# Optimization experiments

Measured on AMD Instinct MI355X. Metric: run time of the kernel, lower is better.

Reference implementation:

```python
import jax, jax.numpy as jnp
import numpy as np

STEPS, K, NEW_PTS, GDIM, HDIM = 10, 64, 1152, 256, 128


def setup_inputs() -> dict:
    key = jax.random.key(0)
    ks = jax.random.split(key, 24)
    def w(k, shape):
        return jax.random.normal(k, shape, dtype=jnp.float32) * 0.02
    inp = {
        'points': jax.random.normal(ks[0], (4, 4096, 3), dtype=jnp.float32),
        'gt': jax.random.normal(ks[1], (4, 4096, 3), dtype=jnp.float32),
        # PointNet encoder: 3->64->128->256 (stored [in,out])
        'enc_w1': w(ks[2], (3, 64)),   'enc_b1': jnp.zeros((64,), jnp.float32),
        'enc_w2': w(ks[3], (64, 128)), 'enc_b2': jnp.zeros((128,), jnp.float32),
        'enc_w3': w(ks[4], (128, GDIM)), 'enc_b3': jnp.zeros((GDIM,), jnp.float32),
        # Attention MLP: (3+256+128)->128->1
        'att_w1': w(ks[5], (3 + GDIM + HDIM, 128)), 'att_b1': jnp.zeros((128,), jnp.float32),
        'att_w2': w(ks[6], (128, 1)), 'att_b2': jnp.zeros((1,), jnp.float32),
        # LSTMCell: input 256+3+3=262, hidden 128, gates i,f,g,o
        'lstm_wih': w(ks[7], (GDIM + 6, 4 * HDIM)), 'lstm_whh': w(ks[8], (HDIM, 4 * HDIM)),
        'lstm_bih': jnp.zeros((4 * HDIM,), jnp.float32), 'lstm_bhh': jnp.zeros((4 * HDIM,), jnp.float32),
        # Refiner: 128->128->new_points*3
        'ref_w1': w(ks[9], (HDIM, 128)), 'ref_b1': jnp.zeros((128,), jnp.float32),
        'ref_w2': w(ks[10], (128, NEW_PTS * 3)), 'ref_b2': jnp.zeros((NEW_PTS * 3,), jnp.float32),
    }
    return inp


def _chamfer_sq(x, y):
    # x: [B,N,3], y: [B,M,3]; squared-L2 chamfer, batch-mean (pytorch3d norm=2)
    d2 = (jnp.sum(x * x, -1)[:, :, None] + jnp.sum(y * y, -1)[:, None, :]
          - 2.0 * jnp.einsum('bnd,bmd->bnm', x, y))  # [B,N,M]
    cd = jnp.mean(jnp.min(d2, axis=2), axis=1) + jnp.mean(jnp.min(d2, axis=1), axis=1)
    return jnp.mean(cd)


def _forward(points, gt, enc_w1, enc_b1, enc_w2, enc_b2, enc_w3, enc_b3,
             att_w1, att_b1, att_w2, att_b2,
             lstm_wih, lstm_whh, lstm_bih, lstm_bhh,
             ref_w1, ref_b1, ref_w2, ref_b2):
    B, N0, _ = points.shape
    h = jnp.zeros((B, HDIM), points.dtype)
    c = jnp.zeros((B, HDIM), points.dtype)
    canvas = points
    for _ in range(STEPS):
        # PointNet encoder + max-pool -> global feature [B,GDIM]
        f = jax.nn.relu(canvas @ enc_w1 + enc_b1)
        f = jax.nn.relu(f @ enc_w2 + enc_b2)
        f = f @ enc_w3 + enc_b3
        gfeat = jnp.max(f, axis=1)
        # attention-weighted centroid
        N = canvas.shape[1]
        ctx = jnp.concatenate([
            canvas,
            jnp.broadcast_to(gfeat[:, None, :], (B, N, GDIM)),
            jnp.broadcast_to(h[:, None, :], (B, N, HDIM)),
        ], axis=-1)
        scores = (jax.nn.relu(ctx @ att_w1 + att_b1) @ att_w2 + att_b2)[..., 0]  # [B,N]
        alpha = jax.nn.softmax(scores, axis=1)
        center = jnp.einsum('bn,bnd->bd', alpha, canvas)
        # brute-force KNN around center + gather
        dist = jnp.linalg.norm(canvas - center[:, None, :], axis=-1)  # [B,N]
        _, idx = jax.lax.top_k(-dist, K)  # smallest K
        patch = jnp.take_along_axis(canvas, idx[:, :, None], axis=1)  # [B,K,3]
        patch_feat = jnp.mean(patch - center[:, None, :], axis=1)  # [B,3]
        # LSTM cell (gate order i,f,g,o)
        lstm_in = jnp.concatenate([gfeat, center, patch_feat], axis=1)
        gates = lstm_in @ lstm_wih + lstm_bih + h @ lstm_whh + lstm_bhh
        gi, gf, gg, go = jnp.split(gates, 4, axis=1)
        c = jax.nn.sigmoid(gf) * c + jax.nn.sigmoid(gi) * jnp.tanh(gg)
        h = jax.nn.sigmoid(go) * jnp.tanh(c)
        # refine: generate new patch points around center
        new_pts = (jax.nn.relu(h @ ref_w1 + ref_b1) @ ref_w2 + ref_b2)
        new_pts = new_pts.reshape(B, NEW_PTS, 3) * 0.02 + center[:, None, :]
        canvas = jnp.concatenate([canvas, new_pts], axis=1)
    p_input = canvas[:, :N0, :]
    p_new = canvas[:, N0:, :]
    total_loss = 0.1 * _chamfer_sq(p_input, gt) + 1.0 * _chamfer_sq(p_new, gt)
    return total_loss


def reference(points, gt, enc_w1, enc_b1, enc_w2, enc_b2, enc_w3, enc_b3,
              att_w1, att_b1, att_w2, att_b2,
              lstm_wih, lstm_whh, lstm_bih, lstm_bhh,
              ref_w1, ref_b1, ref_w2, ref_b2):
    return _forward(points, gt, enc_w1, enc_b1, enc_w2, enc_b2, enc_w3, enc_b3,
                    att_w1, att_b1, att_w2, att_b2,
                    lstm_wih, lstm_whh, lstm_bih, lstm_bhh,
                    ref_w1, ref_b1, ref_w2, ref_b2)
```

## Files before the change

kernel.cpp:

```cpp
#include <hip/hip_runtime.h>
#include <math.h>

#define BB 4
#define N0 4096
#define NEWP 1152
#define GD 256
#define HD 128
#define KSEL 64
#define NSTEPS 10
#define NMAX (N0 + NSTEPS*NEWP)
#define NNEW (NSTEPS*NEWP)

#define OFF_CANVAS 0
#define OFF_MINAB  (OFF_CANVAS + BB*NMAX*3)
#define OFF_MINCD  (OFF_MINAB + 2*BB*N0)
#define OFF_GMAX   (OFF_MINCD + BB*NNEW + BB*N0)
#define OFF_H      (OFF_GMAX + BB*GD)
#define OFF_C      (OFF_H + 2*BB*HD)
#define OFF_ACC    (OFF_C + 2*BB*HD)
#define OFF_CENTER (OFF_ACC + 16)
#define OFF_PART   (OFF_CENTER + 32)
#define OFF_GPART  (OFF_PART + BB*32*8)
#define WS_FLOATS  (OFF_GPART + 32*BB*512)

#define F1S 68
#define F2SD 132

__device__ __forceinline__ unsigned enc_f(float f){
  unsigned u = __float_as_uint(f);
  return (u & 0x80000000u) ? ~u : (u | 0x80000000u);
}
__device__ __forceinline__ float dec_f(unsigned e){
  unsigned u = (e & 0x80000000u) ? (e & 0x7fffffffu) : ~e;
  return __uint_as_float(u);
}
__device__ __forceinline__ float sigm(float x){ return 1.f/(1.f+expf(-x)); }

__device__ __forceinline__ float block_sum(float v, volatile float* red){
#pragma unroll
  for (int s=32;s>0;s>>=1) v += __shfl_down(v, s, 64);
  int lane = threadIdx.x & 63, w = threadIdx.x >> 6, nw = blockDim.x >> 6;
  __syncthreads();
  if (lane==0) red[w] = v;
  __syncthreads();
  if (w==0){
    float x = (lane < nw) ? red[lane] : 0.f;
#pragma unroll
    for (int s=8;s>0;s>>=1) x += __shfl_down(x, s, 64);
    if (lane==0) red[0] = x;
  }
  __syncthreads();
  float r = red[0];
  __syncthreads();
  return r;
}
__device__ __forceinline__ float block_max(float v, volatile float* red){
#pragma unroll
  for (int s=32;s>0;s>>=1) v = fmaxf(v, __shfl_down(v, s, 64));
  int lane = threadIdx.x & 63, w = threadIdx.x >> 6, nw = blockDim.x >> 6;
  __syncthreads();
  if (lane==0) red[w] = v;
  __syncthreads();
  if (w==0){
    float x = (lane < nw) ? red[lane] : -3.4e38f;
#pragma unroll
    for (int s=8;s>0;s>>=1) x = fmaxf(x, __shfl_down(x, s, 64));
    if (lane==0) red[0] = x;
  }
  __syncthreads();
  float r = red[0];
  __syncthreads();
  return r;
}

__device__ __forceinline__ void enc64(
    const float* __restrict__ sP, float* __restrict__ sF1, float* __restrict__ sF2,
    const float* __restrict__ w1, const float* __restrict__ b1,
    const float* __restrict__ w2, const float* __restrict__ b2,
    const float* __restrict__ w3, const float* __restrict__ b3,
    unsigned* __restrict__ gmax_b)
{
  int tid = threadIdx.x;
  int lane = tid & 63;
  int wv = __builtin_amdgcn_readfirstlane(tid >> 6);
#pragma unroll
  for (int k=0;k<8;k++){
    int pt = wv + 8*k;
    float p0 = sP[pt*3], p1 = sP[pt*3+1], p2 = sP[pt*3+2];
    float v = b1[lane] + p0*w1[lane] + p1*w1[64+lane] + p2*w1[128+lane];
    sF1[pt*F1S + lane] = fmaxf(v, 0.f);
  }
  __syncthreads();
  {
    float a[16];
    const float* b2p = b2 + wv*16;
#pragma unroll
    for (int k=0;k<16;k++) a[k] = b2p[k];
#pragma unroll
    for (int kk4=0; kk4<16; kk4++){
      float4 f4 = *(const float4*)&sF1[lane*F1S + kk4*4];
#pragma unroll
      for (int e=0;e<4;e++){
        float fk = ((const float*)&f4)[e];
        const float* wr = w2 + (kk4*4+e)*128 + wv*16;
#pragma unroll
        for (int k=0;k<16;k++) a[k] += fk*wr[k];
      }
    }
#pragma unroll
    for (int k=0;k<16;k++) sF2[lane*F2SD + wv*16 + k] = fmaxf(a[k], 0.f);
  }
  __syncthreads();
  {
    float a3[32];
    const float* b3p = b3 + wv*32;
#pragma unroll
    for (int d=0;d<32;d++) a3[d] = b3p[d];
#pragma unroll 8
    for (int k4=0; k4<32; k4++){
      float4 f4 = *(const float4*)&sF2[lane*F2SD + k4*4];
#pragma unroll
      for (int e=0;e<4;e++){
        float fk = ((const float*)&f4)[e];
        const float* wr = w3 + (k4*4+e)*256 + wv*32;
#pragma unroll
        for (int d=0;d<32;d++) a3[d] += fk*wr[d];
      }
    }
#pragma unroll
    for (int d=0;d<32;d++){
      float v = a3[d];
#pragma unroll
      for (int s=32;s>0;s>>=1) v = fmaxf(v, __shfl_down(v, s, 64));
      if (lane==0) atomicMax(&gmax_b[wv*32 + d], enc_f(v));
    }
  }
}

__global__ __launch_bounds__(512) void init_kernel(
    const float* __restrict__ points,
    float* __restrict__ canvas, unsigned* __restrict__ minAB,
    unsigned* __restrict__ minCD, unsigned* __restrict__ gmax,
    float* __restrict__ h, float* __restrict__ c)
{
  int gid = blockIdx.x*512 + threadIdx.x;
  if (gid < BB*N0*3){
    int b = gid/(N0*3), r = gid - b*(N0*3);
    canvas[(size_t)b*NMAX*3 + r] = points[gid];
  }
  if (gid < 2*BB*N0) minAB[gid] = 0xFFFFFFFFu;
  if (gid < BB*NNEW + BB*N0) minCD[gid] = 0xFFFFFFFFu;
  if (gid < BB*GD) gmax[gid] = 0u;
  if (gid < 2*BB*HD){ h[gid]=0.f; c[gid]=0.f; }
}

__global__ __launch_bounds__(512) void enc_kernel(
    const float* __restrict__ canvas,
    const float* __restrict__ w1, const float* __restrict__ b1,
    const float* __restrict__ w2, const float* __restrict__ b2,
    const float* __restrict__ w3, const float* __restrict__ b3,
    unsigned* __restrict__ gmax)
{
  __shared__ __align__(16) float sP[192];
  __shared__ __align__(16) float sF1[64*F1S];
  __shared__ __align__(16) float sF2[64*F2SD];
  int b = blockIdx.y, lg = blockIdx.x;
  int tid = threadIdx.x;
  if (tid < 192) sP[tid] = canvas[(size_t)b*NMAX*3 + (size_t)lg*192 + tid];
  __syncthreads();
  enc64(sP, sF1, sF2, w1, b1, w2, b2, w3, b3, gmax + b*GD);
}

__global__ __launch_bounds__(512) void sl_kernel(
    const float* __restrict__ canvas, const float* __restrict__ aw1,
    const float* __restrict__ ab1, const float* __restrict__ aw2,
    const float* __restrict__ ab2, const unsigned* __restrict__ gmax,
    const float* __restrict__ h_in,
    const float* __restrict__ wih, const float* __restrict__ whh,
    float* __restrict__ part, float* __restrict__ gpart, int N, int nch)
{
  __shared__ float sBatt[128];
  __shared__ float red[16];
  __shared__ float sV[BB][12];
  int blk = blockIdx.x;
  int tid = threadIdx.x;
  if (blk < 4*nch){
    int b = blk / nch, ch = blk - b*nch;
    if (tid < 128){
      float a = ab1[tid];
      for (int k=0;k<GD;k++) a += dec_f(gmax[b*GD+k]) * aw1[(3+k)*128 + tid];
      for (int k=0;k<HD;k++) a += h_in[b*HD+k] * aw1[(3+GD+k)*128 + tid];
      sBatt[tid] = a;
    }
    __syncthreads();
    int i = ch*512 + tid;
    bool act = i < N;
    float p0=0.f,p1=0.f,p2=0.f,s=-3.4e38f;
    if (act){
      const float* pp = canvas + (size_t)(b*NMAX + i)*3;
      p0=pp[0]; p1=pp[1]; p2=pp[2];
      s = ab2[0];
      for (int j=0;j<128;j++){
        float v = sBatt[j] + p0*aw1[j] + p1*aw1[128+j] + p2*aw1[256+j];
        s += fmaxf(v, 0.f)*aw2[j];
      }
    }
    float mb = block_max(s, red);
    float e = act ? expf(s - mb) : 0.f;
    float se = block_sum(e, red);
    float wx = block_sum(e*p0, red);
    float wy = block_sum(e*p1, red);
    float wz = block_sum(e*p2, red);
    if (tid==0){
      float* pr = part + (size_t)(b*32 + ch)*8;
      pr[0]=mb; pr[1]=se; pr[2]=wx; pr[3]=wy; pr[4]=wz;
    }
  } else {
    int cc = blk - 4*nch;
    if (tid < BB*12){
      int b = tid/12, j = tid - b*12;
      int r = cc*12 + j;
      sV[b][j] = (r < 256) ? dec_f(gmax[b*GD + r]) : h_in[b*HD + (r-256)];
    }
    __syncthreads();
    float a0=0.f,a1=0.f,a2=0.f,a3=0.f;
#pragma unroll
    for (int j=0;j<12;j++){
      int r = cc*12 + j;
      const float* wr = (r < 256) ? (wih + (size_t)r*512) : (whh + (size_t)(r-256)*512);
      float wvv = wr[tid];
      a0 += sV[0][j]*wvv; a1 += sV[1][j]*wvv;
      a2 += sV[2][j]*wvv; a3 += sV[3][j]*wvv;
    }
    float* gp = gpart + (size_t)cc*(BB*512);
    gp[0*512+tid]=a0; gp[1*512+tid]=a1; gp[2*512+tid]=a2; gp[3*512+tid]=a3;
  }
}

__global__ __launch_bounds__(1024) void stepA_kernel(
    const float* __restrict__ canvas, const float* __restrict__ part,
    float* __restrict__ centerpf, int N, int nch)
{
  __shared__ float red[16];
  __shared__ float sC[3];
  __shared__ unsigned cbufA[2][16];
  __shared__ unsigned cbufB[2][16];
  __shared__ int tieCnt;
  __shared__ int tieIdx[256];

  int b = blockIdx.x;
  int tid = threadIdx.x;
  int lane = tid & 63, wid = tid >> 6;
  const float* cv = canvas + (size_t)b*NMAX*3;

  float pm=-3.4e38f, pse=0.f, pwx=0.f, pwy=0.f, pwz=0.f;
  if (tid < nch){
    const float* pp = part + (size_t)(b*32 + tid)*8;
    pm=pp[0]; pse=pp[1]; pwx=pp[2]; pwy=pp[3]; pwz=pp[4];
  }
  float M = block_max(pm, red);
  float w = (tid < nch) ? expf(pm - M) : 0.f;
  float se = block_sum(pse*w, red);
  float wx = block_sum(pwx*w, red);
  float wy = block_sum(pwy*w, red);
  float wz = block_sum(pwz*w, red);
  if (tid==0){ sC[0]=wx/se; sC[1]=wy/se; sC[2]=wz/se; }
  __syncthreads();
  float cx=sC[0], cy=sC[1], cz=sC[2];
  if (tid<3) centerpf[b*3+tid] = sC[tid];

  unsigned ur[16];
#pragma unroll
  for (int q=0;q<16;q++){
    ur[q] = 0xFFFFFFFFu;
    int i = tid + q*1024;
    if (i < N){
      const float* p = cv + (size_t)i*3;
      float dx=p[0]-cx, dy=p[1]-cy, dz=p[2]-cz;
      ur[q] = __float_as_uint(dx*dx + dy*dy + dz*dz);
    }
  }

  unsigned T = 0u;
  int cntBelow = 0;
  int par = 0;
  {
    unsigned cand = 1u<<30;
    unsigned tc = 0;
#pragma unroll
    for (int q=0;q<16;q++) tc += (ur[q] < cand) ? 1u : 0u;
#pragma unroll
    for (int s=32;s>0;s>>=1) tc += __shfl_down(tc, s, 64);
    if (lane==0) cbufA[par][wid] = tc;
    __syncthreads();
    unsigned tot = 0;
#pragma unroll
    for (int i2=0;i2<16;i2++) tot += cbufA[par][i2];
    if ((int)tot < KSEL){ T = cand; cntBelow = (int)tot; }
    par ^= 1;
  }
  for (int bit=29; bit>=1; bit-=2){
    unsigned q1 = 1u<<(bit-1);
    unsigned c1 = T + q1, c2 = T + 2u*q1, c3 = T + 3u*q1;
    unsigned ta = 0, tb = 0;
#pragma unroll
    for (int q=0;q<16;q++){
      unsigned u = ur[q];
      ta += (u < c1 ? 1u : 0u) | (u < c2 ? 0x10000u : 0u);
      tb += (u < c3 ? 1u : 0u);
    }
#pragma unroll
    for (int s=32;s>0;s>>=1){ ta += __shfl_down(ta, s, 64); tb += __shfl_down(tb, s, 64); }
    if (lane==0){ cbufA[par][wid] = ta; cbufB[par][wid] = tb; }
    __syncthreads();
    unsigned sa = 0, sb = 0;
#pragma unroll
    for (int i2=0;i2<16;i2++){ sa += cbufA[par][i2]; sb += cbufB[par][i2]; }
    int n1 = (int)(sa & 0xFFFFu), n2 = (int)(sa >> 16), n3 = (int)sb;
    if (n3 < KSEL){ T = c3; cntBelow = n3; }
    else if (n2 < KSEL){ T = c2; cntBelow = n2; }
    else if (n1 < KSEL){ T = c1; cntBelow = n1; }
    par ^= 1;
  }
  int kneed = KSEL - cntBelow;

  if (tid==0) tieCnt = 0;
  __syncthreads();
  float sx=0.f, sy=0.f, sz=0.f;
#pragma unroll
  for (int q=0;q<16;q++){
    unsigned u = ur[q];
    if (u < T){
      const float* p = cv + (size_t)(tid + q*1024)*3;
      sx += p[0]; sy += p[1]; sz += p[2];
    } else if (u == T){
      int pos = atomicAdd(&tieCnt, 1);
      if (pos < 256) tieIdx[pos] = tid + q*1024;
    }
  }
  __syncthreads();
  sx = block_sum(sx, red);
  sy = block_sum(sy, red);
  sz = block_sum(sz, red);
  if (tid==0){
    int mm = tieCnt < 256 ? tieCnt : 256;
    for (int t=0;t<kneed;t++){
      int best=-1, bi=0x7fffffff;
      for (int q=0;q<mm;q++){ int v = tieIdx[q]; if (v < bi){ bi=v; best=q; } }
      if (best >= 0){
        tieIdx[best] = 0x7fffffff;
        const float* p = cv + (size_t)bi*3;
        sx += p[0]; sy += p[1]; sz += p[2];
      }
    }
    centerpf[16 + b*3 + 0] = sx/KSEL - cx;
    centerpf[16 + b*3 + 1] = sy/KSEL - cy;
    centerpf[16 + b*3 + 2] = sz/KSEL - cz;
  }
}

__global__ __launch_bounds__(512) void refine_enc_kernel(
    float* __restrict__ canvas, const float* __restrict__ gpart,
    const float* __restrict__ centerpf,
    const float* __restrict__ c_in, float* __restrict__ c_out,
    float* __restrict__ h_out,
    const float* __restrict__ wih,
    const float* __restrict__ bih, const float* __restrict__ bhh,
    const float* __restrict__ rw1, const float* __restrict__ rb1,
    const float* __restrict__ rw2, const float* __restrict__ rb2,
    const float* __restrict__ w1, const float* __restrict__ b1,
    const float* __restrict__ w2, const float* __restrict__ b2,
    const float* __restrict__ w3, const float* __restrict__ b3,
    unsigned* __restrict__ gmax, int N)
{
  __shared__ float sG[512];
  __shared__ float sH[HD];
  __shared__ float sRf[HD];
  __shared__ __align__(16) float sP[192];
  __shared__ __align__(16) float sF1[64*F1S];
  __shared__ __align__(16) float sF2[64*F2SD];
  int g = blockIdx.x, b = blockIdx.y;
  int tid = threadIdx.x;
  float cx = centerpf[b*3+0], cy = centerpf[b*3+1], cz = centerpf[b*3+2];
  float fx = centerpf[16+b*3+0], fy = centerpf[16+b*3+1], fz = centerpf[16+b*3+2];
  {
    float gg = bih[tid] + bhh[tid];
    for (int cc=0; cc<32; cc++) gg += gpart[(size_t)cc*(BB*512) + b*512 + tid];
    gg += cx*wih[(size_t)256*512+tid] + cy*wih[(size_t)257*512+tid] + cz*wih[(size_t)258*512+tid];
    gg += fx*wih[(size_t)259*512+tid] + fy*wih[(size_t)260*512+tid] + fz*wih[(size_t)261*512+tid];
    sG[tid] = gg;
  }
  __syncthreads();
  if (tid < HD){
    float gi=sG[tid], gf=sG[128+tid], gg2=sG[256+tid], go=sG[384+tid];
    float cn = sigm(gf)*c_in[b*HD+tid] + sigm(gi)*tanhf(gg2);
    float hn = sigm(go)*tanhf(cn);
    sH[tid] = hn;
    if (g==0){ c_out[b*HD+tid]=cn; h_out[b*HD+tid]=hn; }
  }
  __syncthreads();
  if (tid < HD){
    float a = rb1[tid];
    for (int k=0;k<HD;k++) a += sH[k]*rw1[k*HD + tid];
    sRf[tid] = fmaxf(a, 0.f);
  }
  __syncthreads();
  if (tid < 192){
    int o = g*192 + tid;
    float a = rb2[o];
    for (int k=0;k<HD;k++) a += sRf[k]*rw2[(size_t)k*(NEWP*3) + o];
    float val = a*0.02f + centerpf[b*3 + (tid%3)];
    sP[tid] = val;
    canvas[((size_t)b*NMAX + N)*3 + o] = val;
  }
  __syncthreads();
  enc64(sP, sF1, sF2, w1, b1, w2, b2, w3, b3, gmax + b*GD);
}

__global__ __launch_bounds__(512) void chamfer_kernel(
    const float* __restrict__ canvas, const float* __restrict__ gt,
    unsigned* __restrict__ minAB, unsigned* __restrict__ minCD)
{
  __shared__ float sy0[1024], sy1[1024], sy2[1024], sny[1024];
  int id = blockIdx.x;
  int dir, rem;
  if (id < 32){ dir=0; rem=id; }
  else if (id < 64){ dir=1; rem=id-32; }
  else if (id < 160){ dir=2; rem=id-64; }
  else { dir=3; rem=id-160; }
  int b, xb, yb;
  if (dir < 2){ b = rem>>3; int l = rem&7; xb = l>>2; yb = l&3; }
  else if (dir == 2){ b = rem/24; int l = rem%24; xb = l>>2; yb = l&3; }
  else { b = rem/24; int l = rem%24; xb = l/12; yb = l%12; }

  int Nx, Ny; const float* X; const float* Y; unsigned* mp;
  if (dir==0){      Nx=N0;   Ny=N0;   X=canvas+(size_t)b*NMAX*3;       Y=gt+(size_t)b*N0*3;            mp=minAB + b*N0; }
  else if (dir==1){ Nx=N0;   Ny=N0;   X=gt+(size_t)b*N0*3;             Y=canvas+(size_t)b*NMAX*3;      mp=minAB + BB*N0 + b*N0; }
  else if (dir==2){ Nx=NNEW; Ny=N0;   X=canvas+((size_t)b*NMAX+N0)*3;  Y=gt+(size_t)b*N0*3;            mp=minCD + b*NNEW; }
  else {            Nx=N0;   Ny=NNEW; X=gt+(size_t)b*N0*3;             Y=canvas+((size_t)b*NMAX+N0)*3; mp=minCD + BB*NNEW + b*N0; }

  int xbase = xb*2048;
  int ybase = yb*1024;
  int tn = min(1024, Ny - ybase);
  int tid = threadIdx.x;
  for (int t=tid; t<tn; t+=512){
    const float* yp = Y + (size_t)(ybase+t)*3;
    float y0=yp[0], y1=yp[1], y2=yp[2];
    sy0[t]=y0; sy1[t]=y1; sy2[t]=y2; sny[t]=y0*y0+y1*y1+y2*y2;
  }
  __syncthreads();

  float X0[4],X1[4],X2[4],NXr[4],MN[4]; int XI[4]; bool VA[4];
#pragma unroll
  for (int q=0;q<4;q++){
    int x = xbase + q*512 + tid;
    VA[q] = x < Nx;
    int xc = VA[q] ? x : 0;
    const float* xp = X + (size_t)xc*3;
    X0[q]=xp[0]; X1[q]=xp[1]; X2[q]=xp[2];
    NXr[q] = X0[q]*X0[q] + X1[q]*X1[q] + X2[q]*X2[q];
    MN[q] = 3.4e38f; XI[q] = xc;
  }
  const float4* v0 = (const float4*)sy0;
  const float4* v1 = (const float4*)sy1;
  const float4* v2 = (const float4*)sy2;
  const float4* vn = (const float4*)sny;
  int j4n = tn >> 2;
  for (int j=0;j<j4n;j++){
    float4 a0 = v0[j], a1 = v1[j], a2 = v2[j], an = vn[j];
#pragma unroll
    for (int e=0;e<4;e++){
      float y0 = ((const float*)&a0)[e];
      float y1 = ((const float*)&a1)[e];
      float y2 = ((const float*)&a2)[e];
      float ny = ((const float*)&an)[e];
#pragma unroll
      for (int q=0;q<4;q++){
        float dot = fmaf(X0[q], y0, fmaf(X1[q], y1, X2[q]*y2));
        MN[q] = fminf(MN[q], fmaf(-2.f, dot, ny));
      }
    }
  }
  for (int j=j4n*4; j<tn; j++){
    float y0=sy0[j], y1=sy1[j], y2=sy2[j], ny=sny[j];
#pragma unroll
    for (int q=0;q<4;q++){
      float dot = fmaf(X0[q], y0, fmaf(X1[q], y1, X2[q]*y2));
      MN[q] = fminf(MN[q], fmaf(-2.f, dot, ny));
    }
  }
#pragma unroll
  for (int q=0;q<4;q++)
    if (VA[q]) atomicMin(&mp[XI[q]], enc_f(MN[q] + NXr[q]));
}

__global__ __launch_bounds__(256) void chamfer_reduce_kernel(
    const unsigned* __restrict__ minAB, const unsigned* __restrict__ minCD,
    float* __restrict__ acc)
{
  __shared__ float red[16];
  int s = blockIdx.x, dir = s>>2, b = s&3;
  const unsigned* mp; int len;
  if (dir==0){      mp=minAB + b*N0;            len=N0; }
  else if (dir==1){ mp=minAB + BB*N0 + b*N0;    len=N0; }
  else if (dir==2){ mp=minCD + b*NNEW;          len=NNEW; }
  else {            mp=minCD + BB*NNEW + b*N0;  len=N0; }
  float v = 0.f;
  for (int i=threadIdx.x;i<len;i+=256) v += dec_f(mp[i]);
  v = block_sum(v, red);
  if (threadIdx.x==0) acc[s] = v;
}

__global__ void finish_kernel(const float* __restrict__ acc, float* __restrict__ out)
{
  if (threadIdx.x == 0 && blockIdx.x == 0){
    float cd1 = 0.f, cd2 = 0.f;
    for (int b=0;b<BB;b++) cd1 += acc[b]/(float)N0 + acc[4+b]/(float)N0;
    for (int b=0;b<BB;b++) cd2 += acc[8+b]/(float)NNEW + acc[12+b]/(float)N0;
    out[0] = 0.1f*(cd1/BB) + 1.0f*(cd2/BB);
  }
}

extern "C" void kernel_launch(void* const* d_in, const int* in_sizes, int n_in,
                              void* d_out, int out_size, void* d_ws, size_t ws_size,
                              hipStream_t stream) {
  (void)in_sizes; (void)n_in; (void)out_size; (void)ws_size;
  const float* points   = (const float*)d_in[0];
  const float* gt       = (const float*)d_in[1];
  const float* enc_w1   = (const float*)d_in[2];
  const float* enc_b1   = (const float*)d_in[3];
  const float* enc_w2   = (const float*)d_in[4];
  const float* enc_b2   = (const float*)d_in[5];
  const float* enc_w3   = (const float*)d_in[6];
  const float* enc_b3   = (const float*)d_in[7];
  const float* att_w1   = (const float*)d_in[8];
  const float* att_b1   = (const float*)d_in[9];
  const float* att_w2   = (const float*)d_in[10];
  const float* att_b2   = (const float*)d_in[11];
  const float* lstm_wih = (const float*)d_in[12];
  const float* lstm_whh = (const float*)d_in[13];
  const float* lstm_bih = (const float*)d_in[14];
  const float* lstm_bhh = (const float*)d_in[15];
  const float* ref_w1   = (const float*)d_in[16];
  const float* ref_b1   = (const float*)d_in[17];
  const float* ref_w2   = (const float*)d_in[18];
  const float* ref_b2   = (const float*)d_in[19];
  float* out = (float*)d_out;

  float* ws       = (float*)d_ws;
  float* canvas   = ws + OFF_CANVAS;
  unsigned* minAB = (unsigned*)(ws + OFF_MINAB);
  unsigned* minCD = (unsigned*)(ws + OFF_MINCD);
  unsigned* gmaxp = (unsigned*)(ws + OFF_GMAX);
  float* hb       = ws + OFF_H;
  float* cb       = ws + OFF_C;
  float* acc      = ws + OFF_ACC;
  float* centerb  = ws + OFF_CENTER;
  float* partb    = ws + OFF_PART;
  float* gpartb   = ws + OFF_GPART;

  init_kernel<<<dim3(128), 512, 0, stream>>>(points, canvas, minAB, minCD, gmaxp, hb, cb);
  enc_kernel<<<dim3(64, BB), 512, 0, stream>>>(canvas, enc_w1, enc_b1, enc_w2, enc_b2, enc_w3, enc_b3, gmaxp);

  for (int t=0; t<NSTEPS; t++){
    int N   = N0 + t*NEWP;
    int nch = (N + 511) >> 9;
    float* h_in  = hb + (t&1)*BB*HD;
    float* h_out = hb + ((t+1)&1)*BB*HD;
    float* c_in  = cb + (t&1)*BB*HD;
    float* c_out = cb + ((t+1)&1)*BB*HD;
    sl_kernel<<<dim3(4*nch + 32), 512, 0, stream>>>(canvas, att_w1, att_b1, att_w2, att_b2,
                                                    gmaxp, h_in, lstm_wih, lstm_whh,
                                                    partb, gpartb, N, nch);
    stepA_kernel<<<dim3(BB), 1024, 0, stream>>>(canvas, partb, centerb, N, nch);
    refine_enc_kernel<<<dim3(18, BB), 512, 0, stream>>>(canvas, gpartb, centerb,
                                                        c_in, c_out, h_out,
                                                        lstm_wih, lstm_bih, lstm_bhh,
                                                        ref_w1, ref_b1, ref_w2, ref_b2,
                                                        enc_w1, enc_b1, enc_w2, enc_b2, enc_w3, enc_b3,
                                                        gmaxp, N);
  }

  chamfer_kernel<<<dim3(256), 512, 0, stream>>>(canvas, gt, minAB, minCD);
  chamfer_reduce_kernel<<<dim3(16), 256, 0, stream>>>(minAB, minCD, acc);
  finish_kernel<<<1, 64, 0, stream>>>(acc, out);
}
```

Measured before the change: 1.112 ms.

## Remap PointNet encoder thread work to per-lane points with vector weight loads

The encoder's layer-2 and layer-3 matmuls previously gave each lane one point and each wave a slice of output channels, with per-lane scalar weight reads and a 32-step wave shuffle-max plus atomic for every channel. Now each wave handles 8 points, and each lane computes 4 consecutive output channels per pass, using float4 weight loads and a fixed 4-register accumulator. The max-pool reduces with 3 xor-shuffles across the 8 point lanes, combines waves through a new 8x256 shared buffer, and issues a single atomicMax per channel per block. This cuts atomics and shuffle traffic and lowers register pressure, at the cost of more passes over the shared feature rows, more shared memory and an extra barrier.

```diff
diff --git a/kernel.cpp b/kernel.cpp
--- a/kernel.cpp
+++ b/kernel.cpp
@@ -74,7 +74,8 @@
 }
 
 __device__ __forceinline__ void enc64(
-    const float* __restrict__ sP, float* __restrict__ sF1, float* __restrict__ sF2,
+    const float* __restrict__ sP, float* __restrict__ sF1,
+    float* __restrict__ sF2, float* __restrict__ sRed,
     const float* __restrict__ w1, const float* __restrict__ b1,
     const float* __restrict__ w2, const float* __restrict__ b2,
     const float* __restrict__ w3, const float* __restrict__ b3,
@@ -83,57 +84,75 @@
   int tid = threadIdx.x;
   int lane = tid & 63;
   int wv = __builtin_amdgcn_readfirstlane(tid >> 6);
+  int pg = lane & 7;
+  int dg = lane >> 3;
+  int pt = wv*8 + pg;
+
 #pragma unroll
   for (int k=0;k<8;k++){
-    int pt = wv + 8*k;
-    float p0 = sP[pt*3], p1 = sP[pt*3+1], p2 = sP[pt*3+2];
+    int p = wv + 8*k;
+    float p0 = sP[p*3], p1 = sP[p*3+1], p2 = sP[p*3+2];
     float v = b1[lane] + p0*w1[lane] + p1*w1[64+lane] + p2*w1[128+lane];
-    sF1[pt*F1S + lane] = fmaxf(v, 0.f);
-  }
-  __syncthreads();
-  {
-    float a[16];
-    const float* b2p = b2 + wv*16;
-#pragma unroll
-    for (int k=0;k<16;k++) a[k] = b2p[k];
-#pragma unroll
-    for (int kk4=0; kk4<16; kk4++){
-      float4 f4 = *(const float4*)&sF1[lane*F1S + kk4*4];
+    sF1[p*F1S + lane] = fmaxf(v, 0.f);
+  }
+  __syncthreads();
+
+#pragma unroll
+  for (int jp=0;jp<4;jp++){
+    int j0 = jp*32 + dg*4;
+    float4 bb = *(const float4*)&b2[j0];
+    float a0=bb.x, a1=bb.y, a2=bb.z, a3=bb.w;
+#pragma unroll
+    for (int k4=0;k4<16;k4++){
+      float4 f4 = *(const float4*)&sF1[pt*F1S + k4*4];
 #pragma unroll
       for (int e=0;e<4;e++){
         float fk = ((const float*)&f4)[e];
-        const float* wr = w2 + (kk4*4+e)*128 + wv*16;
-#pragma unroll
-        for (int k=0;k<16;k++) a[k] += fk*wr[k];
+        float4 ww = *(const float4*)&w2[(k4*4+e)*128 + j0];
+        a0 = fmaf(fk, ww.x, a0); a1 = fmaf(fk, ww.y, a1);
+        a2 = fmaf(fk, ww.z, a2); a3 = fmaf(fk, ww.w, a3);
       }
     }
-#pragma unroll
-    for (int k=0;k<16;k++) sF2[lane*F2SD + wv*16 + k] = fmaxf(a[k], 0.f);
-  }
-  __syncthreads();
-  {
-    float a3[32];
-    const float* b3p = b3 + wv*32;
-#pragma unroll
-    for (int d=0;d<32;d++) a3[d] = b3p[d];
-#pragma unroll 8
-    for (int k4=0; k4<32; k4++){
-      float4 f4 = *(const float4*)&sF2[lane*F2SD + k4*4];
+    float4 o;
+    o.x=fmaxf(a0,0.f); o.y=fmaxf(a1,0.f); o.z=fmaxf(a2,0.f); o.w=fmaxf(a3,0.f);
+    *(float4*)&sF2[pt*F2SD + j0] = o;
+  }
+  __syncthreads();
+
+#pragma unroll
+  for (int dp=0;dp<8;dp++){
+    int d0 = dp*32 + dg*4;
+    float4 bb = *(const float4*)&b3[d0];
+    float a0=bb.x, a1=bb.y, a2=bb.z, a3=bb.w;
+#pragma unroll 4
+    for (int k4=0;k4<32;k4++){
+      float4 f4 = *(const float4*)&sF2[pt*F2SD + k4*4];
 #pragma unroll
       for (int e=0;e<4;e++){
         float fk = ((const float*)&f4)[e];
-        const float* wr = w3 + (k4*4+e)*256 + wv*32;
-#pragma unroll
-        for (int d=0;d<32;d++) a3[d] += fk*wr[d];
+        float4 ww = *(const float4*)&w3[(k4*4+e)*256 + d0];
+        a0 = fmaf(fk, ww.x, a0); a1 = fmaf(fk, ww.y, a1);
+        a2 = fmaf(fk, ww.z, a2); a3 = fmaf(fk, ww.w, a3);
       }
     }
 #pragma unroll
-    for (int d=0;d<32;d++){
-      float v = a3[d];
-#pragma unroll
-      for (int s=32;s>0;s>>=1) v = fmaxf(v, __shfl_down(v, s, 64));
-      if (lane==0) atomicMax(&gmax_b[wv*32 + d], enc_f(v));
-    }
+    for (int s=1;s<8;s<<=1){
+      a0 = fmaxf(a0, __shfl_xor(a0, s, 64));
+      a1 = fmaxf(a1, __shfl_xor(a1, s, 64));
+      a2 = fmaxf(a2, __shfl_xor(a2, s, 64));
+      a3 = fmaxf(a3, __shfl_xor(a3, s, 64));
+    }
+    if (pg==0){
+      float4 o; o.x=a0; o.y=a1; o.z=a2; o.w=a3;
+      *(float4*)&sRed[wv*256 + d0] = o;
+    }
+  }
+  __syncthreads();
+  if (tid < 256){
+    float m = sRed[tid];
+#pragma unroll
+    for (int w=1;w<8;w++) m = fmaxf(m, sRed[w*256 + tid]);
+    atomicMax(&gmax_b[tid], enc_f(m));
   }
 }
 
@@ -164,11 +183,12 @@
   __shared__ __align__(16) float sP[192];
   __shared__ __align__(16) float sF1[64*F1S];
   __shared__ __align__(16) float sF2[64*F2SD];
+  __shared__ __align__(16) float sRed[8*256];
   int b = blockIdx.y, lg = blockIdx.x;
   int tid = threadIdx.x;
   if (tid < 192) sP[tid] = canvas[(size_t)b*NMAX*3 + (size_t)lg*192 + tid];
   __syncthreads();
-  enc64(sP, sF1, sF2, w1, b1, w2, b2, w3, b3, gmax + b*GD);
+  enc64(sP, sF1, sF2, sRed, w1, b1, w2, b2, w3, b3, gmax + b*GD);
 }
 
 __global__ __launch_bounds__(512) void sl_kernel(
@@ -379,6 +399,7 @@
   __shared__ __align__(16) float sP[192];
   __shared__ __align__(16) float sF1[64*F1S];
   __shared__ __align__(16) float sF2[64*F2SD];
+  __shared__ __align__(16) float sRed[8*256];
   int g = blockIdx.x, b = blockIdx.y;
   int tid = threadIdx.x;
   float cx = centerpf[b*3+0], cy = centerpf[b*3+1], cz = centerpf[b*3+2];
@@ -414,7 +435,7 @@
     canvas[((size_t)b*NMAX + N)*3 + o] = val;
   }
   __syncthreads();
-  enc64(sP, sF1, sF2, w1, b1, w2, b2, w3, b3, gmax + b*GD);
+  enc64(sP, sF1, sF2, sRed, w1, b1, w2, b2, w3, b3, gmax + b*GD);
 }
 
 __global__ __launch_bounds__(512) void chamfer_kernel(
```

Result: slower. 1.681 ms (+51.3%).
